# Kernel optimization log

Hardware: AMD Instinct MI355X
Metric: run time of the kernel (lower is better)

## Reference

```python
import jax, jax.numpy as jnp
import numpy as np


def _lstm(x, Wih, Whh, bih, bhh):
    # x: [T,B,E] -> outputs [T,B,H]; torch gate order i,f,g,o
    B = x.shape[1]
    H = Whh.shape[1]
    bias = bih + bhh
    def step(carry, xt):
        h, c = carry
        g = xt @ Wih.T + h @ Whh.T + bias  # [B,4H]
        i, f, gg, o = jnp.split(g, 4, axis=-1)
        c = jax.nn.sigmoid(f) * c + jax.nn.sigmoid(i) * jnp.tanh(gg)
        h = jax.nn.sigmoid(o) * jnp.tanh(c)
        return (h, c), h
    init = (jnp.zeros((B, H), x.dtype), jnp.zeros((B, H), x.dtype))
    _, hs = jax.lax.scan(step, init, x)
    return hs


def setup_inputs():
    key = jax.random.key(0)
    ks = jax.random.split(key, 16)
    B, T, V, NT, E, H = 128, 512, 50000, 24, 128, 256
    Hd = H // 2  # per-direction hidden
    s = 0.08
    x = jax.random.randint(ks[0], (B, T), 0, V)
    tags = jax.random.randint(ks[1], (B, T), 0, NT)
    lengths = jax.random.randint(ks[2], (B,), T // 2, T + 1)
    mask = jnp.arange(T)[None, :] < lengths[:, None]  # [B,T] bool, position 0 always valid
    emb = (jax.random.normal(ks[3], (V, E)) * s).at[0].set(0.0)  # padding_idx=0 row zeroed
    Wih_f = jax.random.normal(ks[4], (4 * Hd, E)) * s
    Whh_f = jax.random.normal(ks[5], (4 * Hd, Hd)) * s
    bih_f = jax.random.normal(ks[6], (4 * Hd,)) * s
    bhh_f = jax.random.normal(ks[7], (4 * Hd,)) * s
    Wih_b = jax.random.normal(ks[8], (4 * Hd, E)) * s
    Whh_b = jax.random.normal(ks[9], (4 * Hd, Hd)) * s
    bih_b = jax.random.normal(ks[10], (4 * Hd,)) * s
    bhh_b = jax.random.normal(ks[11], (4 * Hd,)) * s
    W_out = jax.random.normal(ks[12], (NT, H)) * s
    b_out = jnp.zeros((NT,))
    transitions = jax.random.normal(ks[13], (NT, NT))
    start_trans = jax.random.normal(ks[14], (NT,))
    end_trans = jax.random.normal(ks[15], (NT,))
    return {"x": x, "tags": tags, "mask": mask, "emb": emb,
            "Wih_f": Wih_f, "Whh_f": Whh_f, "bih_f": bih_f, "bhh_f": bhh_f,
            "Wih_b": Wih_b, "Whh_b": Whh_b, "bih_b": bih_b, "bhh_b": bhh_b,
            "W_out": W_out, "b_out": b_out, "transitions": transitions,
            "start_trans": start_trans, "end_trans": end_trans}


def reference(x, tags, mask, emb, Wih_f, Whh_f, bih_f, bhh_f,
              Wih_b, Whh_b, bih_b, bhh_b, W_out, b_out,
              transitions, start_trans, end_trans):
    # --- emissions (dropout is identity in eval) ---
    xe = emb[x]                       # [B,T,E]
    xt = xe.transpose(1, 0, 2)        # [T,B,E]
    hf = _lstm(xt, Wih_f, Whh_f, bih_f, bhh_f)               # [T,B,Hd]
    hb = _lstm(xt[::-1], Wih_b, Whh_b, bih_b, bhh_b)[::-1]   # [T,B,Hd]
    h = jnp.concatenate([hf, hb], axis=-1).transpose(1, 0, 2)  # [B,T,H]
    emissions = h @ W_out.T + b_out   # [B,T,NT]

    # --- CRF forward algorithm (logZ) via scan over time ---
    score0 = start_trans + emissions[:, 0]  # [B,NT]
    em_rest = emissions[:, 1:].transpose(1, 0, 2)  # [T-1,B,NT]
    m_rest = mask[:, 1:].T                        # [T-1,B]
    def fwd_step(score, inp):
        em_t, m_t = inp
        ns = jax.nn.logsumexp(score[:, :, None] + transitions[None] + em_t[:, None, :], axis=1)
        return jnp.where(m_t[:, None], ns, score), None
    score, _ = jax.lax.scan(fwd_step, score0, (em_rest, m_rest))
    logZ = jax.nn.logsumexp(score + end_trans, axis=1)  # [B]

    # --- gold path score, fully vectorized ---
    mf = mask.astype(emissions.dtype)
    emit = jnp.take_along_axis(emissions, tags[:, :, None], axis=2)[:, :, 0]  # [B,T]
    trans = transitions[tags[:, :-1], tags[:, 1:]]                            # [B,T-1]
    gold = start_trans[tags[:, 0]] + emit[:, 0] + jnp.sum((trans + emit[:, 1:]) * mf[:, 1:], axis=1)
    last_idx = mask.sum(axis=1) - 1
    last_tags = jnp.take_along_axis(tags, last_idx[:, None], axis=1)[:, 0]
    gold = gold + end_trans[last_tags]

    return jnp.mean(logZ - gold)
```

## Files before the change

### kernel.cpp

```cpp
#include <hip/hip_runtime.h>
#include <hip/hip_bf16.h>

typedef unsigned short u16;
typedef unsigned int   u32;
typedef _Float16 half2_t __attribute__((ext_vector_type(2)));
typedef short    bf16x8 __attribute__((ext_vector_type(8)));
typedef float    f32x4  __attribute__((ext_vector_type(4)));
typedef u32      u32x4v __attribute__((ext_vector_type(4)));

#define TT   512

__device__ __forceinline__ float sigf(float x)  { return 1.0f / (1.0f + __expf(-x)); }
__device__ __forceinline__ float tanhf_(float x){ return 1.0f - 2.0f / (__expf(2.0f * x) + 1.0f); }

__device__ __forceinline__ u16 f2bf(float x) {
  __hip_bfloat16 h = __float2bfloat16(x);
  return *reinterpret_cast<u16*>(&h);
}
__device__ __forceinline__ float bf2f(u16 u) { return __uint_as_float(((u32)u) << 16); }
__device__ __forceinline__ u32 pk2(float a, float b) {
  return (u32)f2bf(a) | ((u32)f2bf(b) << 16);
}
__device__ __forceinline__ u16 f2h(float x) {
  _Float16 h = (_Float16)x;
  union { _Float16 f; u16 u; } c; c.f = h; return c.u;
}
__device__ __forceinline__ half2_t u2h2(u32 v) {
  union { u32 u; half2_t h; } c; c.u = v; return c.h;
}

__global__ __launch_bounds__(256) void prep_k(
    const float* __restrict__ Wih_f, const float* __restrict__ Wih_b,
    const float* __restrict__ Whh_f, const float* __restrict__ Whh_b,
    const float* __restrict__ bih_f, const float* __restrict__ bhh_f,
    const float* __restrict__ bih_b, const float* __restrict__ bhh_b,
    const float* __restrict__ W_out,
    u16* __restrict__ Wb, u16* __restrict__ Whhb, float* __restrict__ bias,
    u32* __restrict__ Wout16)
{
  int i = blockIdx.x * 256 + threadIdx.x;
  {
    int n = i >> 7, k = i & 127;
    int d = n >> 9, rem = n & 511, uu = rem >> 2, g = rem & 3;
    const float* W = d ? Wih_b : Wih_f;
    Wb[i] = f2bf(W[(g * 128 + uu) * 128 + k]);
  }
  {
    int d = i >> 16, rem = i & 65535, n = rem >> 7, k = rem & 127;
    const float* W = d ? Whh_b : Whh_f;
    Whhb[i] = f2bf(W[n * 128 + k]);
  }
  if (i < 1024) {
    int d = i >> 9, rem = i & 511, uu = rem >> 2, g = rem & 3;
    int src = g * 128 + uu;
    bias[i] = d ? (bih_b[src] + bhh_b[src]) : (bih_f[src] + bhh_f[src]);
  }
  if (i < 3072) {
    Wout16[i] = (u32)f2h(W_out[2 * i]) | ((u32)f2h(W_out[2 * i + 1]) << 16);
  }
}

__global__ __launch_bounds__(256) void embed_k(
    const int* __restrict__ x, const float* __restrict__ emb, u16* __restrict__ xe)
{
  const int tid = threadIdx.x;
  const int r = blockIdx.x * 8 + (tid >> 5);
  const int lane = tid & 31;
  int token = x[r];
  float4 v = *(const float4*)&emb[(size_t)token * 128 + lane * 4];
  uint2 p; p.x = pk2(v.x, v.y); p.y = pk2(v.z, v.w);
  *(uint2*)&xe[(size_t)r * 128 + lane * 4] = p;
}

__global__ __launch_bounds__(256, 2) void gates_mfma_k(
    const u16* __restrict__ xe, const u16* __restrict__ Wb,
    const float* __restrict__ bias, u16* __restrict__ Gout)
{
  const int tid = threadIdx.x;
  const int wid = tid >> 6, l = tid & 63;
  const int wm = wid >> 1, wn = wid & 1;
  const int M0 = blockIdx.y * 128, N0 = blockIdx.x * 128;
  const int lr = l & 15, lk = l >> 4;

  f32x4 acc[4][4];
#pragma unroll
  for (int i = 0; i < 4; ++i)
#pragma unroll
    for (int j = 0; j < 4; ++j) acc[i][j] = (f32x4){0.f, 0.f, 0.f, 0.f};

#pragma unroll
  for (int ks = 0; ks < 4; ++ks) {
    bf16x8 a[4], b[4];
#pragma unroll
    for (int mi = 0; mi < 4; ++mi)
      a[mi] = *(const bf16x8*)&xe[(size_t)(M0 + wm * 64 + mi * 16 + lr) * 128 + ks * 32 + lk * 8];
#pragma unroll
    for (int ni = 0; ni < 4; ++ni)
      b[ni] = *(const bf16x8*)&Wb[(size_t)(N0 + wn * 64 + ni * 16 + lr) * 128 + ks * 32 + lk * 8];
#pragma unroll
    for (int mi = 0; mi < 4; ++mi)
#pragma unroll
      for (int ni = 0; ni < 4; ++ni)
        acc[mi][ni] = __builtin_amdgcn_mfma_f32_16x16x32_bf16(a[mi], b[ni], acc[mi][ni], 0, 0, 0);
  }

  float bcol[4];
#pragma unroll
  for (int ni = 0; ni < 4; ++ni) bcol[ni] = bias[N0 + wn * 64 + ni * 16 + lr];

  __shared__ u16 cs[128][136];
#pragma unroll
  for (int mi = 0; mi < 4; ++mi)
#pragma unroll
    for (int ni = 0; ni < 4; ++ni) {
      int col = wn * 64 + ni * 16 + lr;
#pragma unroll
      for (int r = 0; r < 4; ++r) {
        int row = wm * 64 + mi * 16 + lk * 4 + r;
        cs[row][col] = f2bf(acc[mi][ni][r] + bcol[ni]);
      }
    }
  __syncthreads();
  {
    int row = tid >> 1, c0 = (tid & 1) * 64;
    u16* dst = &Gout[(size_t)(M0 + row) * 1024 + N0 + c0];
#pragma unroll
    for (int q = 0; q < 8; ++q)
      *(uint4*)&dst[q * 8] = *(const uint4*)&cs[row][c0 + q * 8];
  }
}

__global__ __launch_bounds__(512, 1) void lstm_mfma_k(
    const u16* __restrict__ G, const u16* __restrict__ Whhb,
    u16* __restrict__ Hout)
{
  const int bid = blockIdx.x;
  const int dir = bid >> 7;
  const int b   = bid & 127;
  const int tid = threadIdx.x;
  const int w = tid >> 6, l = tid & 63;
  const int lr = l & 15, lk = l >> 4;
  const int u = 16 * w + lr;

  const u16* wbase = Whhb + ((size_t)dir << 16);
  bf16x8 B[4][4];
#pragma unroll
  for (int g = 0; g < 4; ++g)
#pragma unroll
    for (int ks = 0; ks < 4; ++ks)
      B[g][ks] = *(const bf16x8*)&wbase[(size_t)(g * 128 + u) * 128 + ks * 32 + lk * 8];

  __shared__ u16 hl[2][16][136];

  for (int i = tid; i < 2 * 16 * 136; i += 512) ((u16*)hl)[i] = 0;

  float cc = 0.f;
  const int ts = dir ? -1 : 1;
  const int t0 = dir ? (TT - 1) : 0;
  const long gstride = (long)ts * 1024;
  const long hstride = (long)ts * 256;

  const u16* gptr = G + ((size_t)b * 512 + t0) * 1024 + dir * 512 + u * 4;
  u16*       hptr = Hout + ((size_t)b * 512 + t0) * 256 + dir * 128 + u;

  ushort4 qa[8], qb[8];
#pragma unroll
  for (int j = 0; j < 8; ++j)
    qa[j] = *(const ushort4*)(gptr + j * gstride);
  const u16* gpf = gptr + 8 * gstride;

  u16 hprev = 0;
  __syncthreads();

#define LSTM_STEP(Q, P, DOSTORE) { \
    if (DOSTORE) { if (lk == 0) *hptr = hprev; hptr += hstride; } \
    bf16x8 A[4]; \
    _Pragma("unroll") \
    for (int ks = 0; ks < 4; ++ks) \
      A[ks] = *(const bf16x8*)&hl[P][lr][ks * 32 + lk * 8]; \
    f32x4 ac0 = (f32x4){0.f,0.f,0.f,0.f}, ac1 = (f32x4){0.f,0.f,0.f,0.f}; \
    f32x4 ac2 = (f32x4){0.f,0.f,0.f,0.f}, ac3 = (f32x4){0.f,0.f,0.f,0.f}; \
    _Pragma("unroll") \
    for (int ks = 0; ks < 4; ++ks) { \
      ac0 = __builtin_amdgcn_mfma_f32_16x16x32_bf16(A[ks], B[0][ks], ac0, 0, 0, 0); \
      ac1 = __builtin_amdgcn_mfma_f32_16x16x32_bf16(A[ks], B[1][ks], ac1, 0, 0, 0); \
      ac2 = __builtin_amdgcn_mfma_f32_16x16x32_bf16(A[ks], B[2][ks], ac2, 0, 0, 0); \
      ac3 = __builtin_amdgcn_mfma_f32_16x16x32_bf16(A[ks], B[3][ks], ac3, 0, 0, 0); \
    } \
    if (lk == 0) { \
      float gi = ac0[0] + bf2f((Q).x); \
      float gf = ac1[0] + bf2f((Q).y); \
      float gg = ac2[0] + bf2f((Q).z); \
      float go = ac3[0] + bf2f((Q).w); \
      float iv = sigf(gi), fv = sigf(gf), gv = tanhf_(gg), ov = sigf(go); \
      cc = fv * cc + iv * gv; \
      float hv = ov * tanhf_(cc); \
      hl[(P) ^ 1][0][u] = f2bf(hv); \
      hprev = f2h(hv); \
    } \
    __syncthreads(); }

#define LSTM_CHUNK(QC, QN, DOLOAD, FIRST) { \
    if (DOLOAD) { \
      _Pragma("unroll") \
      for (int j = 0; j < 8; ++j) \
        QN[j] = *(const ushort4*)(gpf + j * gstride); \
      gpf += 8 * gstride; \
    } \
    LSTM_STEP(QC[0], 0, !(FIRST)) \
    LSTM_STEP(QC[1], 1, true) \
    LSTM_STEP(QC[2], 0, true) \
    LSTM_STEP(QC[3], 1, true) \
    LSTM_STEP(QC[4], 0, true) \
    LSTM_STEP(QC[5], 1, true) \
    LSTM_STEP(QC[6], 0, true) \
    LSTM_STEP(QC[7], 1, true) }

  LSTM_CHUNK(qa, qb, true, true)
  for (int p = 0; p < 31; ++p) {
    LSTM_CHUNK(qb, qa, true, false)
    LSTM_CHUNK(qa, qb, true, false)
  }
  LSTM_CHUNK(qb, qa, false, false)

#undef LSTM_CHUNK
#undef LSTM_STEP

  if (lk == 0) *hptr = hprev;
}

__global__ __launch_bounds__(256) void emis_k(
    const u16* __restrict__ Hb, const u32* __restrict__ Wout16,
    const float* __restrict__ b_out, float* __restrict__ em)
{
  __shared__ __align__(16) u32 wl2[24 * 128];
  __shared__ float bo[24];
  const int tid = threadIdx.x;
  for (int i = tid; i < 3072; i += 256) wl2[i] = Wout16[i];
  if (tid < 24) bo[tid] = b_out[tid];
  __syncthreads();

  const int m = blockIdx.x * 256 + tid;
  float acc[24];
#pragma unroll
  for (int tg = 0; tg < 24; ++tg) acc[tg] = bo[tg];

  const u32* h2 = (const u32*)(Hb + (size_t)m * 256);
  for (int ck = 0; ck < 16; ++ck) {
    uint4 hv = *(const uint4*)(h2 + ck * 4);
#pragma unroll
    for (int tg = 0; tg < 24; ++tg) {
      u32x4v wv = *(const u32x4v*)&wl2[tg * 128 + ck * 4];
      float a = acc[tg];
      a = __builtin_amdgcn_fdot2(u2h2(hv.x), u2h2(wv.x), a, false);
      a = __builtin_amdgcn_fdot2(u2h2(hv.y), u2h2(wv.y), a, false);
      a = __builtin_amdgcn_fdot2(u2h2(hv.z), u2h2(wv.z), a, false);
      a = __builtin_amdgcn_fdot2(u2h2(hv.w), u2h2(wv.w), a, false);
      acc[tg] = a;
    }
  }
#pragma unroll
  for (int t6 = 0; t6 < 6; ++t6) {
    float4 o;
    o.x = acc[t6*4+0]; o.y = acc[t6*4+1]; o.z = acc[t6*4+2]; o.w = acc[t6*4+3];
    *(float4*)&em[(size_t)m * 24 + t6 * 4] = o;
  }
}

__device__ __forceinline__ int get_mask(const void* mp, int idx, bool byte_mode) {
  return byte_mode ? (int)((const unsigned char*)mp)[idx] : ((const int*)mp)[idx];
}

__global__ __launch_bounds__(64) void crf_k(
    const float* __restrict__ em, const int* __restrict__ tags,
    const void* __restrict__ maskp, const float* __restrict__ trans,
    const float* __restrict__ start_tr, const float* __restrict__ end_tr,
    float* __restrict__ out)
{
  const int b = blockIdx.x;
  const int tid = threadIdx.x;
  const bool byte_mode = (*(const u32*)maskp != 1u);
  const bool act = (tid < 48);
  const int j  = (tid < 24) ? tid : (act ? tid - 24 : 0);
  const int i0 = (tid < 24) ? 0 : 12;
  const int partner = (tid < 24) ? tid + 24 : tid - 24;

  int cnt = 0;
  for (int t = tid; t < TT; t += 64) cnt += get_mask(maskp, b * TT + t, byte_mode);
#pragma unroll
  for (int off = 32; off > 0; off >>= 1) cnt += __shfl_down(cnt, off);
  cnt = __shfl(cnt, 0);

  float Texp[12];
  if (act) {
#pragma unroll
    for (int k = 0; k < 12; ++k) Texp[k] = __expf(trans[(i0 + k) * 24 + j]);
  } else {
#pragma unroll
    for (int k = 0; k < 12; ++k) Texp[k] = 0.f;
  }

  float sc0 = act ? (start_tr[j] + em[(size_t)(b * TT) * 24 + j]) : -1e30f;
  float m = sc0;
#pragma unroll
  for (int off = 32; off > 0; off >>= 1) m = fmaxf(m, __shfl_xor(m, off));
  float P = act ? __expf(sc0 - m) : 0.f;
  float logC = m;

  float em_next = 0.f;
  if (act && cnt > 1) em_next = em[(size_t)(b * TT + 1) * 24 + j];

  for (int t = 1; t < cnt; ++t) {
    float em_cur = em_next;
    if (act && t + 1 < cnt) em_next = em[(size_t)(b * TT + t + 1) * 24 + j];

    float s0 = 0.f, s1 = 0.f, s2 = 0.f;
#pragma unroll
    for (int k = 0; k < 4; ++k)  s0 += __shfl(P, i0 + k)     * Texp[k];
#pragma unroll
    for (int k = 4; k < 8; ++k)  s1 += __shfl(P, i0 + k)     * Texp[k];
#pragma unroll
    for (int k = 8; k < 12; ++k) s2 += __shfl(P, i0 + k)     * Texp[k];
    float sh = (s0 + s1) + s2;
    float so = __shfl(sh, partner);
    float tot = sh + so;
    P = act ? (__expf(em_cur) * tot) : 0.f;

    if ((t & 3) == 0) {
      float mm = P;
#pragma unroll
      for (int off = 32; off > 0; off >>= 1) mm = fmaxf(mm, __shfl_xor(mm, off));
      P = P / mm;
      logC += __logf(mm);
    }
  }

  float z = (tid < 24) ? P * __expf(end_tr[tid]) : 0.f;
#pragma unroll
  for (int off = 32; off > 0; off >>= 1) z += __shfl_xor(z, off);
  float lzv = logC + __logf(z);

  float part = 0.f;
  for (int t = tid; t < TT; t += 64) {
    if (t >= 1 && t < cnt) {
      int tp = tags[b * TT + t - 1], tc = tags[b * TT + t];
      part += trans[tp * 24 + tc] + em[((size_t)(b * TT + t)) * 24 + tc];
    }
  }
#pragma unroll
  for (int off = 32; off > 0; off >>= 1) part += __shfl_down(part, off);
  if (tid == 0) {
    int t0g = tags[b * TT];
    float gold = start_tr[t0g] + em[(size_t)(b * TT) * 24 + t0g] + part;
    gold += end_tr[tags[b * TT + cnt - 1]];
    atomicAdd(out, (lzv - gold) * (1.0f / 128.0f));
  }
}

extern "C" void kernel_launch(void* const* d_in, const int* in_sizes, int n_in,
                              void* d_out, int out_size, void* d_ws, size_t ws_size,
                              hipStream_t stream) {
  const int*   x     = (const int*)d_in[0];
  const int*   tags  = (const int*)d_in[1];
  const void*  mask  = d_in[2];
  const float* emb   = (const float*)d_in[3];
  const float* Wih_f = (const float*)d_in[4];
  const float* Whh_f = (const float*)d_in[5];
  const float* bih_f = (const float*)d_in[6];
  const float* bhh_f = (const float*)d_in[7];
  const float* Wih_b = (const float*)d_in[8];
  const float* Whh_b = (const float*)d_in[9];
  const float* bih_b = (const float*)d_in[10];
  const float* bhh_b = (const float*)d_in[11];
  const float* W_out = (const float*)d_in[12];
  const float* b_out = (const float*)d_in[13];
  const float* trans = (const float*)d_in[14];
  const float* st_tr = (const float*)d_in[15];
  const float* en_tr = (const float*)d_in[16];

  u16*   Gb     = (u16*)d_ws;
  u16*   Hb     = Gb + (size_t)65536 * 1024;
  float* em     = (float*)(Hb + (size_t)65536 * 256);
  float* bias   = em + (size_t)65536 * 24;
  u16*   Wb     = (u16*)(bias + 1024);
  u16*   Whhb   = Wb + 131072;
  u32*   Wout16 = (u32*)(Whhb + 131072);
  u16*   xe     = Hb;

  prep_k<<<512, 256, 0, stream>>>(Wih_f, Wih_b, Whh_f, Whh_b,
                                  bih_f, bhh_f, bih_b, bhh_b, W_out,
                                  Wb, Whhb, bias, Wout16);
  embed_k<<<8192, 256, 0, stream>>>(x, emb, xe);
  gates_mfma_k<<<dim3(8, 512), 256, 0, stream>>>(xe, Wb, bias, Gb);
  lstm_mfma_k<<<256, 512, 0, stream>>>(Gb, Whhb, Hb);
  emis_k<<<256, 256, 0, stream>>>(Hb, Wout16, b_out, em);
  (void)hipMemsetAsync(d_out, 0, sizeof(float), stream);
  crf_k<<<128, 64, 0, stream>>>(em, tags, mask, trans, st_tr, en_tr, (float*)d_out);
}
```

Before: 606.1 us.

## Replace MFMA LSTM recurrence with per-thread fp16 dot2 gate rows

Result: slower. 631.2 us (+4.2%).

```diff
diff --git a/kernel.cpp b/kernel.cpp
--- a/kernel.cpp
+++ b/kernel.cpp
@@ -35,7 +35,7 @@
     const float* __restrict__ bih_f, const float* __restrict__ bhh_f,
     const float* __restrict__ bih_b, const float* __restrict__ bhh_b,
     const float* __restrict__ W_out,
-    u16* __restrict__ Wb, u16* __restrict__ Whhb, float* __restrict__ bias,
+    u16* __restrict__ Wb, u32* __restrict__ Whh16, float* __restrict__ bias,
     u32* __restrict__ Wout16)
 {
   int i = blockIdx.x * 256 + threadIdx.x;
@@ -45,10 +45,13 @@
     const float* W = d ? Wih_b : Wih_f;
     Wb[i] = f2bf(W[(g * 128 + uu) * 128 + k]);
   }
-  {
-    int d = i >> 16, rem = i & 65535, n = rem >> 7, k = rem & 127;
+  if (i < 65536) {
+    int d = i >> 15, rem = i & 32767, n = rem >> 6, kp = rem & 63;
+    int uu = n >> 2, g = n & 3;
     const float* W = d ? Whh_b : Whh_f;
-    Whhb[i] = f2bf(W[n * 128 + k]);
+    float f0 = W[(g * 128 + uu) * 128 + 2 * kp];
+    float f1 = W[(g * 128 + uu) * 128 + 2 * kp + 1];
+    Whh16[i] = (u32)f2h(f0) | ((u32)f2h(f1) << 16);
   }
   if (i < 1024) {
     int d = i >> 9, rem = i & 511, uu = rem >> 2, g = rem & 3;
@@ -130,29 +133,30 @@
   }
 }
 
-__global__ __launch_bounds__(512, 1) void lstm_mfma_k(
-    const u16* __restrict__ G, const u16* __restrict__ Whhb,
+__global__ __launch_bounds__(512, 2) void lstm_dot_k(
+    const u16* __restrict__ G, const u32* __restrict__ Whh16,
     u16* __restrict__ Hout)
 {
   const int bid = blockIdx.x;
   const int dir = bid >> 7;
   const int b   = bid & 127;
   const int tid = threadIdx.x;
-  const int w = tid >> 6, l = tid & 63;
-  const int lr = l & 15, lk = l >> 4;
-  const int u = 16 * w + lr;
-
-  const u16* wbase = Whhb + ((size_t)dir << 16);
-  bf16x8 B[4][4];
-#pragma unroll
-  for (int g = 0; g < 4; ++g)
-#pragma unroll
-    for (int ks = 0; ks < 4; ++ks)
-      B[g][ks] = *(const bf16x8*)&wbase[(size_t)(g * 128 + u) * 128 + ks * 32 + lk * 8];
-
-  __shared__ u16 hl[2][16][136];
-
-  for (int i = tid; i < 2 * 16 * 136; i += 512) ((u16*)hl)[i] = 0;
+  const int u   = tid >> 2;
+  const bool own = (tid & 3) == 0;
+  const bool gg2 = (tid & 3) == 2;
+
+  u32 w[64];
+  {
+    const u32* wrow = Whh16 + ((size_t)dir << 15) + (size_t)tid * 64;
+#pragma unroll
+    for (int q4 = 0; q4 < 16; ++q4) {
+      u32x4v v = *(const u32x4v*)(wrow + 4 * q4);
+      w[4*q4+0] = v.x; w[4*q4+1] = v.y; w[4*q4+2] = v.z; w[4*q4+3] = v.w;
+    }
+  }
+
+  __shared__ __align__(16) u16 hs[2][128];
+  if (tid < 256) ((u16*)hs)[tid] = 0;
 
   float cc = 0.f;
   const int ts = dir ? -1 : 1;
@@ -160,42 +164,40 @@
   const long gstride = (long)ts * 1024;
   const long hstride = (long)ts * 256;
 
-  const u16* gptr = G + ((size_t)b * 512 + t0) * 1024 + dir * 512 + u * 4;
+  const u16* gptr = G + ((size_t)b * 512 + t0) * 1024 + dir * 512 + tid;
   u16*       hptr = Hout + ((size_t)b * 512 + t0) * 256 + dir * 128 + u;
 
-  ushort4 qa[8], qb[8];
-#pragma unroll
-  for (int j = 0; j < 8; ++j)
-    qa[j] = *(const ushort4*)(gptr + j * gstride);
+  u16 qa[8], qb[8];
+#pragma unroll
+  for (int j = 0; j < 8; ++j) qa[j] = gptr[j * gstride];
   const u16* gpf = gptr + 8 * gstride;
 
   u16 hprev = 0;
   __syncthreads();
 
-#define LSTM_STEP(Q, P, DOSTORE) { \
-    if (DOSTORE) { if (lk == 0) *hptr = hprev; hptr += hstride; } \
-    bf16x8 A[4]; \
+#define LSTM_STEP(QW, P, DOSTORE) { \
+    if (DOSTORE) { if (own) *hptr = hprev; hptr += hstride; } \
+    float a0 = 0.f, a1 = 0.f, a2 = 0.f, a3 = 0.f; \
+    const uint4* hb4 = (const uint4*)hs[P]; \
     _Pragma("unroll") \
-    for (int ks = 0; ks < 4; ++ks) \
-      A[ks] = *(const bf16x8*)&hl[P][lr][ks * 32 + lk * 8]; \
-    f32x4 ac0 = (f32x4){0.f,0.f,0.f,0.f}, ac1 = (f32x4){0.f,0.f,0.f,0.f}; \
-    f32x4 ac2 = (f32x4){0.f,0.f,0.f,0.f}, ac3 = (f32x4){0.f,0.f,0.f,0.f}; \
-    _Pragma("unroll") \
-    for (int ks = 0; ks < 4; ++ks) { \
-      ac0 = __builtin_amdgcn_mfma_f32_16x16x32_bf16(A[ks], B[0][ks], ac0, 0, 0, 0); \
-      ac1 = __builtin_amdgcn_mfma_f32_16x16x32_bf16(A[ks], B[1][ks], ac1, 0, 0, 0); \
-      ac2 = __builtin_amdgcn_mfma_f32_16x16x32_bf16(A[ks], B[2][ks], ac2, 0, 0, 0); \
-      ac3 = __builtin_amdgcn_mfma_f32_16x16x32_bf16(A[ks], B[3][ks], ac3, 0, 0, 0); \
+    for (int qq = 0; qq < 16; ++qq) { \
+      uint4 hv4 = hb4[qq]; \
+      asm("v_dot2_f32_f16 %0, %1, %2, %0" : "+v"(a0) : "v"(hv4.x), "v"(w[4*qq+0])); \
+      asm("v_dot2_f32_f16 %0, %1, %2, %0" : "+v"(a1) : "v"(hv4.y), "v"(w[4*qq+1])); \
+      asm("v_dot2_f32_f16 %0, %1, %2, %0" : "+v"(a2) : "v"(hv4.z), "v"(w[4*qq+2])); \
+      asm("v_dot2_f32_f16 %0, %1, %2, %0" : "+v"(a3) : "v"(hv4.w), "v"(w[4*qq+3])); \
     } \
-    if (lk == 0) { \
-      float gi = ac0[0] + bf2f((Q).x); \
-      float gf = ac1[0] + bf2f((Q).y); \
-      float gg = ac2[0] + bf2f((Q).z); \
-      float go = ac3[0] + bf2f((Q).w); \
-      float iv = sigf(gi), fv = sigf(gf), gv = tanhf_(gg), ov = sigf(go); \
-      cc = fv * cc + iv * gv; \
-      float hv = ov * tanhf_(cc); \
-      hl[(P) ^ 1][0][u] = f2bf(hv); \
+    float v = bf2f(QW) + ((a0 + a1) + (a2 + a3)); \
+    float y = gg2 ? (2.f * v) : v; \
+    float s = 1.0f / (1.0f + __expf(-y)); \
+    float a = gg2 ? (2.f * s - 1.f) : s; \
+    float x1 = __shfl_xor(a, 1); \
+    float x2 = __shfl_xor(a, 2); \
+    float x3 = __shfl_xor(a, 3); \
+    if (own) { \
+      cc = x1 * cc + a * x2; \
+      float hv = x3 * tanhf_(cc); \
+      hs[(P) ^ 1][u] = f2h(hv); \
       hprev = f2h(hv); \
     } \
     __syncthreads(); }
@@ -203,8 +205,7 @@
 #define LSTM_CHUNK(QC, QN, DOLOAD, FIRST) { \
     if (DOLOAD) { \
       _Pragma("unroll") \
-      for (int j = 0; j < 8; ++j) \
-        QN[j] = *(const ushort4*)(gpf + j * gstride); \
+      for (int j = 0; j < 8; ++j) QN[j] = gpf[j * gstride]; \
       gpf += 8 * gstride; \
     } \
     LSTM_STEP(QC[0], 0, !(FIRST)) \
@@ -226,7 +227,7 @@
 #undef LSTM_CHUNK
 #undef LSTM_STEP
 
-  if (lk == 0) *hptr = hprev;
+  if (own) *hptr = hprev;
 }
 
 __global__ __launch_bounds__(256) void emis_k(
@@ -383,16 +384,16 @@
   float* em     = (float*)(Hb + (size_t)65536 * 256);
   float* bias   = em + (size_t)65536 * 24;
   u16*   Wb     = (u16*)(bias + 1024);
-  u16*   Whhb   = Wb + 131072;
-  u32*   Wout16 = (u32*)(Whhb + 131072);
+  u32*   Whh16  = (u32*)(Wb + 131072);
+  u32*   Wout16 = Whh16 + 65536;
   u16*   xe     = Hb;
 
   prep_k<<<512, 256, 0, stream>>>(Wih_f, Wih_b, Whh_f, Whh_b,
                                   bih_f, bhh_f, bih_b, bhh_b, W_out,
-                                  Wb, Whhb, bias, Wout16);
+                                  Wb, Whh16, bias, Wout16);
   embed_k<<<8192, 256, 0, stream>>>(x, emb, xe);
   gates_mfma_k<<<dim3(8, 512), 256, 0, stream>>>(xe, Wb, bias, Gb);
-  lstm_mfma_k<<<256, 512, 0, stream>>>(Gb, Whhb, Hb);
+  lstm_dot_k<<<256, 512, 0, stream>>>(Gb, Whh16, Hb);
   emis_k<<<256, 256, 0, stream>>>(Hb, Wout16, b_out, em);
   (void)hipMemsetAsync(d_out, 0, sizeof(float), stream);
   crf_k<<<128, 64, 0, stream>>>(em, tags, mask, trans, st_tr, en_tr, (float*)d_out);
```
